# Kernel optimization log

Measured on AMD Instinct MI355X. Metric: run time of the kernel, lower is better.

Reference implementation:

```python
import jax, jax.numpy as jnp
import numpy as np

WS = (2, 7, 7)   # window size (d, h, w)
NH = 4           # num heads
EPS = 1e-5       # LayerNorm eps (torch default)


def _rel_index():
    wd, wh, ww = WS
    coords = np.stack(np.meshgrid(np.arange(wd), np.arange(wh), np.arange(ww), indexing='ij'))  # (3,wd,wh,ww)
    cf = coords.reshape(3, -1)                      # (3, N)
    rel = cf[:, :, None] - cf[:, None, :]           # (3, N, N)
    rel = rel.transpose(1, 2, 0).astype(np.int64)   # (N, N, 3)
    rel[..., 0] += wd - 1
    rel[..., 1] += wh - 1
    rel[..., 2] += ww - 1
    rel[..., 0] *= (2 * wh - 1) * (2 * ww - 1)
    rel[..., 1] *= (2 * ww - 1)
    return jnp.asarray(rel.sum(-1), dtype=jnp.int32)  # (N, N)


def setup_inputs() -> dict:
    key = jax.random.key(0)
    ks = jax.random.split(key, 6)
    C, CH = 128, 512
    TBL = (2 * WS[0] - 1) * (2 * WS[1] - 1) * (2 * WS[2] - 1)  # 507
    rn = lambda k, s, sc=0.02: jax.random.normal(k, s, jnp.float32) * sc
    return {
        'x': jax.random.normal(ks[0], (2, 8, 56, 56, C), jnp.float32),
        'norm1_w': jnp.ones((C,), jnp.float32), 'norm1_b': jnp.zeros((C,), jnp.float32),
        'qkv_w': rn(ks[1], (3 * C, C)), 'qkv_b': jnp.zeros((3 * C,), jnp.float32),
        'bias_table': rn(ks[2], (TBL, NH)),
        'proj_w': rn(ks[3], (C, C)), 'proj_b': jnp.zeros((C,), jnp.float32),
        'norm2_w': jnp.ones((C,), jnp.float32), 'norm2_b': jnp.zeros((C,), jnp.float32),
        'fc1_w': rn(ks[4], (CH, C)), 'fc1_b': jnp.zeros((CH,), jnp.float32),
        'fc2_w': rn(ks[5], (C, CH)), 'fc2_b': jnp.zeros((C,), jnp.float32),
        'rel_index': _rel_index(),
    }


def _layernorm(x, w, b):
    m = jnp.mean(x, axis=-1, keepdims=True)
    v = jnp.mean(jnp.square(x - m), axis=-1, keepdims=True)
    return (x - m) * jax.lax.rsqrt(v + EPS) * w + b


def reference(x, norm1_w, norm1_b, qkv_w, qkv_b, bias_table, proj_w, proj_b,
              norm2_w, norm2_b, fc1_w, fc1_b, fc2_w, fc2_b, rel_index):
    B, D, H, W, C = x.shape
    wd, wh, ww = WS
    N = wd * wh * ww
    hd = C // NH

    shortcut = x
    xn = _layernorm(x, norm1_w, norm1_b)
    # window partition: (B,D,H,W,C) -> (B*nW, N, C)
    xw = xn.reshape(B, D // wd, wd, H // wh, wh, W // ww, ww, C)
    xw = xw.transpose(0, 1, 3, 5, 2, 4, 6, 7).reshape(-1, N, C)
    B_ = xw.shape[0]

    qkv = (xw @ qkv_w.T + qkv_b).reshape(B_, N, 3, NH, hd).transpose(2, 0, 3, 1, 4)
    q, k, v = qkv[0] * (hd ** -0.5), qkv[1], qkv[2]   # (B_, NH, N, hd)
    attn = jnp.einsum('bhnd,bhmd->bhnm', q, k)
    bias = bias_table[rel_index.reshape(-1)].reshape(N, N, NH).transpose(2, 0, 1)  # (NH,N,N)
    attn = jax.nn.softmax(attn + bias[None], axis=-1)
    out = jnp.einsum('bhnm,bhmd->bhnd', attn, v).transpose(0, 2, 1, 3).reshape(B_, N, C)
    out = out @ proj_w.T + proj_b

    # window reverse: (B*nW, N, C) -> (B,D,H,W,C)
    xr = out.reshape(B, D // wd, H // wh, W // ww, wd, wh, ww, C)
    xr = xr.transpose(0, 1, 4, 2, 5, 3, 6, 7).reshape(B, D, H, W, C)

    x = shortcut + xr
    h = _layernorm(x, norm2_w, norm2_b)
    h = jax.nn.gelu(h @ fc1_w.T + fc1_b, approximate=False)  # torch nn.GELU = exact erf
    return x + (h @ fc2_w.T + fc2_b)
```

## Files before the change

kernel.cpp:

```cpp
#include <hip/hip_runtime.h>
#include <hip/hip_bf16.h>

typedef __hip_bfloat16 bf16;
typedef unsigned short u16t;
typedef unsigned int u32t;
typedef __attribute__((ext_vector_type(8))) short bf16x8_t;
typedef __attribute__((ext_vector_type(4))) float f32x4_t;

#define DEVI static __device__ __forceinline__

DEVI float u2f(u32t bits) { union { u32t u; float f; } v; v.u = bits; return v.f; }
DEVI float bflo(u32t u) { return u2f((u & 0xffffu) << 16); }
DEVI float bfhi(u32t u) { return u2f(u & 0xffff0000u); }
DEVI float sh2f(short s) { return u2f(((u32t)(u16t)s) << 16); }
DEVI float bf2f(bf16 h) { return __bfloat162float(h); }
DEVI bf16 f2bf(float f) { return __float2bfloat16(f); }
DEVI u16t f2bfbits(float f) {
  bf16 h = __float2bfloat16(f);
  union { bf16 h; u16t u; } v; v.h = h; return v.u;
}

DEVI void gl_lds16(const void* g, void* l) {
  __builtin_amdgcn_global_load_lds(
      (const __attribute__((address_space(1))) unsigned int*)g,
      (__attribute__((address_space(3))) unsigned int*)l, 16, 0, 0);
}

#define TOK   50176
#define NWIN  512
#define NTOK  98
#define NHEAD 4
#define HDIM  32
#define QSCALE 0.17677669529663687f

__global__ __launch_bounds__(256) void cvt4_k(
    const float* __restrict__ a, const float* __restrict__ b,
    const float* __restrict__ c, const float* __restrict__ d,
    bf16* __restrict__ o) {
  int i = blockIdx.x * 256 + threadIdx.x;
  const float* s; int off;
  if (i < 49152)       { s = a; off = 0; }
  else if (i < 65536)  { s = b; off = 49152; }
  else if (i < 131072) { s = c; off = 65536; }
  else                 { s = d; off = 131072; }
  float v = s[i - off];
  if (i < 16384) v *= QSCALE;
  o[i] = f2bf(v);
}

__global__ __launch_bounds__(256) void bias_k(const float* __restrict__ btab,
                                              const int* __restrict__ relidx,
                                              const float* __restrict__ qkv_b,
                                              float* __restrict__ BmatT,
                                              float* __restrict__ bsc) {
  int idx = blockIdx.x * 256 + threadIdx.x;
  if (idx < NTOK * NTOK) {
    int i = idx / NTOK, j = idx - i * NTOK;
    int r = relidx[idx] * NHEAD;
#pragma unroll
    for (int h = 0; h < NHEAD; h++)
      BmatT[(size_t)(h * NTOK + j) * 112 + i] = btab[r + h];
  }
  if (blockIdx.x == 0 && threadIdx.x < 384)
    bsc[threadIdx.x] = qkv_b[threadIdx.x] * (threadIdx.x < 128 ? QSCALE : 1.0f);
}

__global__ __launch_bounds__(256) void ln1_k(
    const float* __restrict__ x, const float* __restrict__ w,
    const float* __restrict__ b, bf16* __restrict__ o)
{
  const int wave = threadIdx.x >> 6, lane = threadIdx.x & 63;
  const int t = blockIdx.x * 4 + wave;
  const int c = lane << 1;
  float2 xv = *(const float2*)(x + (size_t)t * 128 + c);
  float x0 = xv.x, x1 = xv.y;
  float s = x0 + x1, ss = x0 * x0 + x1 * x1;
#pragma unroll
  for (int m = 32; m; m >>= 1) { s += __shfl_xor(s, m); ss += __shfl_xor(ss, m); }
  float mean = s * 0.0078125f;
  float var = ss * 0.0078125f - mean * mean;
  float rstd = rsqrtf(var + 1e-5f);
  float y0 = (x0 - mean) * rstd * w[c]     + b[c];
  float y1 = (x1 - mean) * rstd * w[c + 1] + b[c + 1];
  int wi = t % 56; int r = t / 56;
  int hi_ = r % 56; r /= 56;
  int di = r & 7; int bi = r >> 3;
  int nw = ((bi * 4 + (di >> 1)) * 8 + hi_ / 7) * 8 + wi / 7;
  int n  = ((di & 1) * 7 + hi_ % 7) * 7 + wi % 7;
  u32t ov = ((u32t)f2bfbits(y1) << 16) | (u32t)f2bfbits(y0);
  *(u32t*)((u16t*)o + (size_t)(nw * NTOK + n) * 128 + c) = ov;
}

DEVI int winrev(int grow) {
  int nw = grow / NTOK, n = grow - nw * NTOK;
  int wq = nw & 7, hq = (nw >> 3) & 7, dq = (nw >> 6) & 3, bb = nw >> 8;
  int wr = n % 7; int q7 = n / 7; int hr = q7 % 7, dr = q7 / 7;
  return ((bb * 8 + dq * 2 + dr) * 56 + hq * 7 + hr) * 56 + wq * 7 + wr;
}

template <int MODE, int NT16, int KT>
__global__ __launch_bounds__(256) void gemm3_k(
    const bf16* __restrict__ A, const bf16* __restrict__ W,
    const float* __restrict__ bias, const float* __restrict__ resX,
    const bf16* __restrict__ resB2, bf16* __restrict__ outB,
    bf16* __restrict__ outB2, float* __restrict__ outF,
    const float* __restrict__ lnw, const float* __restrict__ lnb, int N)
{
  __shared__ __align__(16) short As[128 * 128];
  __shared__ __align__(16) short Bs[NT16 * 16 * 128];
  const int K = KT * 128;
  const int tid = threadIdx.x;
  const int rowBase = blockIdx.y << 7;
  const int colBase = blockIdx.x * (NT16 * 16);
  const int wv = tid >> 6, lane = tid & 63;
  const int q = lane >> 4, r16 = lane & 15;
  const int mB = wv << 5;

  f32x4_t acc[2][NT16];
#pragma unroll
  for (int i = 0; i < 2; i++)
#pragma unroll
    for (int j = 0; j < NT16; j++) acc[i][j] = (f32x4_t){0.f, 0.f, 0.f, 0.f};

#pragma unroll
  for (int kt = 0; kt < KT; kt++) {
    const int kc = kt << 7;
#pragma unroll
    for (int t = 0; t < 8; t++) {
      int f = tid + (t << 8);
      int row = f >> 4, cs = (f & 15) ^ (row & 15);
      gl_lds16((const u16t*)A + (size_t)(rowBase + row) * K + kc + (cs << 3),
               &As[f << 3]);
    }
#pragma unroll
    for (int t = 0; t < NT16; t++) {
      int f = tid + (t << 8);
      int row = f >> 4, cs = (f & 15) ^ (row & 15);
      gl_lds16((const u16t*)W + (size_t)(colBase + row) * K + kc + (cs << 3),
               &Bs[f << 3]);
    }
    __syncthreads();
#pragma unroll
    for (int ks = 0; ks < 4; ks++) {
      bf16x8_t af[2], bfr[NT16];
#pragma unroll
      for (int mt = 0; mt < 2; mt++) {
        int row = mB + (mt << 4) + r16;
        int slot = ((ks << 2) + q) ^ (row & 15);
        af[mt] = *(const bf16x8_t*)&As[(row << 7) + (slot << 3)];
      }
#pragma unroll
      for (int nt = 0; nt < NT16; nt++) {
        int row = (nt << 4) + r16;
        int slot = ((ks << 2) + q) ^ (row & 15);
        bfr[nt] = *(const bf16x8_t*)&Bs[(row << 7) + (slot << 3)];
      }
#pragma unroll
      for (int mt = 0; mt < 2; mt++)
#pragma unroll
        for (int nt = 0; nt < NT16; nt++)
          acc[mt][nt] = __builtin_amdgcn_mfma_f32_16x16x32_bf16(
              af[mt], bfr[nt], acc[mt][nt], 0, 0, 0);
    }
    __syncthreads();
  }

  float bv[NT16];
#pragma unroll
  for (int nt = 0; nt < NT16; nt++) bv[nt] = bias[colBase + (nt << 4) + r16];

  if (MODE == 1) {
#pragma unroll
    for (int mt = 0; mt < 2; mt++)
#pragma unroll
      for (int reg = 0; reg < 4; reg++) {
        int lrow = mB + (mt << 4) + (q << 2) + reg;
#pragma unroll
        for (int nt = 0; nt < NT16; nt++)
          As[(lrow << 7) + (nt << 4) + r16] = (short)f2bfbits(acc[mt][nt][reg] + bv[nt]);
      }
    __syncthreads();
#pragma unroll
    for (int t = 0; t < 8; t++) {
      int f = tid + (t << 8);
      int row = f >> 4, c8 = (f & 15) << 3;
      int tt = winrev(rowBase + row);
      size_t ob = (size_t)tt * 128 + c8;
      float4 r0 = *(const float4*)(resX + ob);
      float4 r1 = *(const float4*)(resX + ob + 4);
      short* cs = &As[(row << 7) + c8];
      u16t pk[8];
      pk[0] = f2bfbits(sh2f(cs[0]) + r0.x); pk[1] = f2bfbits(sh2f(cs[1]) + r0.y);
      pk[2] = f2bfbits(sh2f(cs[2]) + r0.z); pk[3] = f2bfbits(sh2f(cs[3]) + r0.w);
      pk[4] = f2bfbits(sh2f(cs[4]) + r1.x); pk[5] = f2bfbits(sh2f(cs[5]) + r1.y);
      pk[6] = f2bfbits(sh2f(cs[6]) + r1.z); pk[7] = f2bfbits(sh2f(cs[7]) + r1.w);
      *(uint4*)((u16t*)outB + ob) = *(const uint4*)pk;
      *(uint4*)cs = *(const uint4*)pk;
    }
    __syncthreads();
    const int c = lane << 1;
    float2 lw = *(const float2*)(lnw + c);
    float2 lb = *(const float2*)(lnb + c);
#pragma unroll 4
    for (int rr = 0; rr < 32; rr++) {
      int row = (wv << 5) + rr;
      u32t u = *(const u32t*)&As[(row << 7) + c];
      float x0 = bflo(u), x1 = bfhi(u);
      float s = x0 + x1, ss = x0 * x0 + x1 * x1;
#pragma unroll
      for (int m = 32; m; m >>= 1) { s += __shfl_xor(s, m); ss += __shfl_xor(ss, m); }
      float mean = s * 0.0078125f;
      float var = ss * 0.0078125f - mean * mean;
      float rstd = rsqrtf(var + 1e-5f);
      float y0 = (x0 - mean) * rstd * lw.x + lb.x;
      float y1 = (x1 - mean) * rstd * lw.y + lb.y;
      int tt = winrev(rowBase + row);
      u32t ov = ((u32t)f2bfbits(y1) << 16) | (u32t)f2bfbits(y0);
      *(u32t*)((u16t*)outB2 + (size_t)tt * 128 + c) = ov;
    }
    return;
  }

#pragma unroll
  for (int mt = 0; mt < 2; mt++)
#pragma unroll
    for (int reg = 0; reg < 4; reg++) {
      int lrow = mB + (mt << 4) + (q << 2) + reg;
#pragma unroll
      for (int nt = 0; nt < NT16; nt++) {
        float v = acc[mt][nt][reg] + bv[nt];
        As[(lrow << 6) + (nt << 4) + r16] = (short)f2bfbits(v);
      }
    }
  __syncthreads();
#pragma unroll
  for (int t = 0; t < 4; t++) {
    int f = tid + (t << 8);
    int row = f >> 3, c8 = (f & 7) << 3;
    size_t ob = (size_t)(rowBase + row) * N + colBase + c8;
    *(uint4*)((u16t*)outB + ob) = *(const uint4*)&As[(row << 6) + c8];
  }
}

__global__ __launch_bounds__(256, 2) void mlp_fused_k(
    const bf16* __restrict__ Axn, const bf16* __restrict__ F1,
    const bf16* __restrict__ F2, const float* __restrict__ b1,
    const float* __restrict__ b2, const bf16* __restrict__ resB,
    float* __restrict__ out)
{
  __shared__ __align__(16) char smem[81920];
  short* As  = (short*)smem;
  short* F1s = (short*)(smem + 32768);
  short* F2s = (short*)(smem + 49152);
  short* Hs  = (short*)(smem + 65536);
  float* Cf  = (float*)smem;

  const int tid = threadIdx.x;
  const int rowBase = blockIdx.x << 7;
  const int wv = tid >> 6, lane = tid & 63;
  const int q = lane >> 4, r16 = lane & 15;
  const int mB = wv << 5;

#pragma unroll
  for (int t = 0; t < 8; t++) {
    int f = tid + (t << 8);
    int row = f >> 4, cs = (f & 15) ^ (row & 15);
    gl_lds16((const u16t*)Axn + (size_t)(rowBase + row) * 128 + (cs << 3),
             &As[f << 3]);
  }
#pragma unroll
  for (int t = 0; t < 4; t++) {
    int f = tid + (t << 8);
    int row = f >> 4, cs = (f & 15) ^ (row & 15);
    gl_lds16((const u16t*)F1 + (size_t)row * 128 + (cs << 3), &F1s[f << 3]);
  }
#pragma unroll
  for (int t = 0; t < 4; t++) {
    int f = tid + (t << 8);
    int row = f >> 3, cs = (f & 7) ^ (row & 7);
    gl_lds16((const u16t*)F2 + (size_t)row * 512 + (cs << 3), &F2s[f << 3]);
  }
  __syncthreads();

  f32x4_t oacc[2][8];
#pragma unroll
  for (int i = 0; i < 2; i++)
#pragma unroll
    for (int j = 0; j < 8; j++) oacc[i][j] = (f32x4_t){0.f, 0.f, 0.f, 0.f};

#pragma unroll 1
  for (int c = 0; c < 8; c++) {
    if (c > 0) {
#pragma unroll
      for (int t = 0; t < 4; t++) {
        int f = tid + (t << 8);
        int row = f >> 4, cs = (f & 15) ^ (row & 15);
        gl_lds16((const u16t*)F1 + (size_t)(c * 64 + row) * 128 + (cs << 3),
                 &F1s[f << 3]);
      }
#pragma unroll
      for (int t = 0; t < 4; t++) {
        int f = tid + (t << 8);
        int row = f >> 3, cs = (f & 7) ^ (row & 7);
        gl_lds16((const u16t*)F2 + (size_t)row * 512 + c * 64 + (cs << 3),
                 &F2s[f << 3]);
      }
      __syncthreads();
    }

    f32x4_t hacc[2][4];
#pragma unroll
    for (int i = 0; i < 2; i++)
#pragma unroll
      for (int j = 0; j < 4; j++) hacc[i][j] = (f32x4_t){0.f, 0.f, 0.f, 0.f};
#pragma unroll
    for (int ks = 0; ks < 4; ks++) {
      bf16x8_t af[2], bfr[4];
#pragma unroll
      for (int mt = 0; mt < 2; mt++) {
        int row = mB + (mt << 4) + r16;
        int slot = ((ks << 2) + q) ^ (row & 15);
        af[mt] = *(const bf16x8_t*)&As[(row << 7) + (slot << 3)];
      }
#pragma unroll
      for (int nt = 0; nt < 4; nt++) {
        int row = (nt << 4) + r16;
        int slot = ((ks << 2) + q) ^ (row & 15);
        bfr[nt] = *(const bf16x8_t*)&F1s[(row << 7) + (slot << 3)];
      }
#pragma unroll
      for (int mt = 0; mt < 2; mt++)
#pragma unroll
        for (int nt = 0; nt < 4; nt++)
          hacc[mt][nt] = __builtin_amdgcn_mfma_f32_16x16x32_bf16(
              af[mt], bfr[nt], hacc[mt][nt], 0, 0, 0);
    }

    float bb[4];
#pragma unroll
    for (int nt = 0; nt < 4; nt++) bb[nt] = b1[c * 64 + (nt << 4) + r16];
#pragma unroll
    for (int mt = 0; mt < 2; mt++)
#pragma unroll
      for (int reg = 0; reg < 4; reg++) {
        int lrow = mB + (mt << 4) + (q << 2) + reg;
#pragma unroll
        for (int nt = 0; nt < 4; nt++) {
          float v = hacc[mt][nt][reg] + bb[nt];
          v = 0.5f * v * (1.0f + erff(v * 0.70710678118654752f));
          int col = (nt << 4) + r16;
          int sp = (col >> 3) ^ (lrow & 7);
          Hs[(lrow << 6) + (sp << 3) + (col & 7)] = (short)f2bfbits(v);
        }
      }
    __syncthreads();

#pragma unroll
    for (int ks = 0; ks < 2; ks++) {
      bf16x8_t af[2], bfr[8];
#pragma unroll
      for (int mt = 0; mt < 2; mt++) {
        int row = mB + (mt << 4) + r16;
        int slot = ((ks << 2) + q) ^ (row & 7);
        af[mt] = *(const bf16x8_t*)&Hs[(row << 6) + (slot << 3)];
      }
#pragma unroll
      for (int nt = 0; nt < 8; nt++) {
        int row = (nt << 4) + r16;
        int slot = ((ks << 2) + q) ^ (row & 7);
        bfr[nt] = *(const bf16x8_t*)&F2s[(row << 6) + (slot << 3)];
      }
#pragma unroll
      for (int mt = 0; mt < 2; mt++)
#pragma unroll
        for (int nt = 0; nt < 8; nt++)
          oacc[mt][nt] = __builtin_amdgcn_mfma_f32_16x16x32_bf16(
              af[mt], bfr[nt], oacc[mt][nt], 0, 0, 0);
    }
    __syncthreads();
  }

  float bv[8];
#pragma unroll
  for (int nt = 0; nt < 8; nt++) bv[nt] = b2[(nt << 4) + r16];
#pragma unroll
  for (int mt = 0; mt < 2; mt++)
#pragma unroll
    for (int reg = 0; reg < 4; reg++) {
      int lrow = mB + (mt << 4) + (q << 2) + reg;
#pragma unroll
      for (int nt = 0; nt < 8; nt++)
        Cf[lrow * 132 + (nt << 4) + r16] = oacc[mt][nt][reg] + bv[nt];
    }
  __syncthreads();
#pragma unroll
  for (int t = 0; t < 16; t++) {
    int f = tid + (t << 8);
    int row = f >> 5, c4 = (f & 31) << 2;
    size_t ob = (size_t)(rowBase + row) * 128 + c4;
    const u16t* rp = (const u16t*)resB + ob;
    const float* cp = &Cf[row * 132 + c4];
    float4 v;
    v.x = cp[0] + sh2f(rp[0]);
    v.y = cp[1] + sh2f(rp[1]);
    v.z = cp[2] + sh2f(rp[2]);
    v.w = cp[3] + sh2f(rp[3]);
    *(float4*)(out + ob) = v;
  }
}

#define PSTR 136
__global__ __launch_bounds__(256) void attn_mfma_k(
    const bf16* __restrict__ qkv, const float* __restrict__ BmatT,
    bf16* __restrict__ out)
{
  __shared__ short Vt[32 * PSTR];
  __shared__ short Ps[112 * PSTR];
  const int nw = blockIdx.x, h = blockIdx.y;
  const int tid = threadIdx.x;
  const int wv = tid >> 6, lane = tid & 63;
  const int q = lane >> 4, r16 = lane & 15;

  for (int idx = tid; idx < 32 * 38; idx += 256) {
    int d = idx / 38, j = 98 + idx % 38;
    Vt[d * PSTR + j] = 0;
  }
  for (int idx = tid; idx < 112 * 12; idx += 256) {
    int r = idx / 12, c = (idx % 12) << 1;
    *(u32t*)&Ps[r * PSTR + 112 + c] = 0;
  }
  for (int idx = tid; idx < NTOK * 16; idx += 256) {
    int j = idx >> 4, d2 = (idx & 15) << 1;
    u32t uv = *(const u32t*)((const u16t*)qkv +
                             (size_t)(nw * NTOK + j) * 384 + 256 + h * 32 + d2);
    Vt[d2 * PSTR + j] = (short)(uv & 0xffffu);
    Vt[(d2 + 1) * PSTR + j] = (short)(uv >> 16);
  }
  __syncthreads();

  const int mt0 = wv;
  const bool has2 = (wv + 4) < 7;
  const int mt1 = has2 ? wv + 4 : wv;

  int i0 = mt0 * 16 + r16; if (i0 > NTOK - 1) i0 = NTOK - 1;
  int i1 = mt1 * 16 + r16; if (i1 > NTOK - 1) i1 = NTOK - 1;
  bf16x8_t aq0 = *(const bf16x8_t*)((const u16t*)qkv +
      (size_t)(nw * NTOK + i0) * 384 + h * 32 + (q << 3));
  bf16x8_t aq1 = *(const bf16x8_t*)((const u16t*)qkv +
      (size_t)(nw * NTOK + i1) * 384 + h * 32 + (q << 3));

  f32x4_t sc[2][7];
#pragma unroll
  for (int nt = 0; nt < 7; nt++) {
    int j = (nt << 4) + r16; if (j > NTOK - 1) j = NTOK - 1;
    const float* bRow = &BmatT[(size_t)(h * NTOK + j) * 112];
    bf16x8_t bk = *(const bf16x8_t*)((const u16t*)qkv +
        (size_t)(nw * NTOK + j) * 384 + 128 + h * 32 + (q << 3));
    f32x4_t b0 = *(const f32x4_t*)&bRow[mt0 * 16 + (q << 2)];
    f32x4_t b1 = *(const f32x4_t*)&bRow[mt1 * 16 + (q << 2)];
    sc[0][nt] = __builtin_amdgcn_mfma_f32_16x16x32_bf16(aq0, bk, b0, 0, 0, 0);
    sc[1][nt] = __builtin_amdgcn_mfma_f32_16x16x32_bf16(aq1, bk, b1, 0, 0, 0);
  }

#pragma unroll
  for (int sel = 0; sel < 2; sel++) {
    if (sel == 1 && !has2) break;
    int mtile = sel ? mt1 : mt0;
    int ibase = mtile * 16 + (q << 2);
    float s[4][7];
#pragma unroll
    for (int nt = 0; nt < 7; nt++) {
      int j = (nt << 4) + r16;
#pragma unroll
      for (int reg = 0; reg < 4; reg++) {
        int i = ibase + reg;
        s[reg][nt] = (i < NTOK && j < NTOK) ? sc[sel][nt][reg] : -1.0e30f;
      }
    }
#pragma unroll
    for (int reg = 0; reg < 4; reg++) {
      float m = -3.0e38f;
#pragma unroll
      for (int nt = 0; nt < 7; nt++) m = fmaxf(m, s[reg][nt]);
#pragma unroll
      for (int d = 8; d; d >>= 1) m = fmaxf(m, __shfl_xor(m, d));
      float sum = 0.f;
#pragma unroll
      for (int nt = 0; nt < 7; nt++) { s[reg][nt] = __expf(s[reg][nt] - m); sum += s[reg][nt]; }
#pragma unroll
      for (int d = 8; d; d >>= 1) sum += __shfl_xor(sum, d);
      float inv = 1.f / sum;
#pragma unroll
      for (int nt = 0; nt < 7; nt++)
        Ps[(ibase + reg) * PSTR + (nt << 4) + r16] =
            (short)f2bfbits(s[reg][nt] * inv);
    }
    f32x4_t o0 = {0.f, 0.f, 0.f, 0.f}, o1 = {0.f, 0.f, 0.f, 0.f};
#pragma unroll
    for (int kt = 0; kt < 4; kt++) {
      bf16x8_t ap = *(const bf16x8_t*)&Ps[(mtile * 16 + r16) * PSTR + (kt << 5) + (q << 3)];
      bf16x8_t bv0 = *(const bf16x8_t*)&Vt[r16 * PSTR + (kt << 5) + (q << 3)];
      bf16x8_t bv1 = *(const bf16x8_t*)&Vt[(16 + r16) * PSTR + (kt << 5) + (q << 3)];
      o0 = __builtin_amdgcn_mfma_f32_16x16x32_bf16(ap, bv0, o0, 0, 0, 0);
      o1 = __builtin_amdgcn_mfma_f32_16x16x32_bf16(ap, bv1, o1, 0, 0, 0);
    }
#pragma unroll
    for (int reg = 0; reg < 4; reg++) {
      int i = mtile * 16 + (q << 2) + reg;
      if (i < NTOK) {
        size_t ob = (size_t)(nw * NTOK + i) * 128 + h * 32;
        out[ob + r16] = f2bf(o0[reg]);
        out[ob + 16 + r16] = f2bf(o1[reg]);
      }
    }
  }
}

extern "C" void kernel_launch(void* const* d_in, const int* in_sizes, int n_in,
                              void* d_out, int out_size, void* d_ws, size_t ws_size,
                              hipStream_t stream) {
  const float* x      = (const float*)d_in[0];
  const float* n1w    = (const float*)d_in[1];
  const float* n1b    = (const float*)d_in[2];
  const float* qkv_w  = (const float*)d_in[3];
  const float* qkv_b  = (const float*)d_in[4];
  const float* btab   = (const float*)d_in[5];
  const float* proj_w = (const float*)d_in[6];
  const float* proj_b = (const float*)d_in[7];
  const float* n2w    = (const float*)d_in[8];
  const float* n2b    = (const float*)d_in[9];
  const float* fc1_w  = (const float*)d_in[10];
  const float* fc1_b  = (const float*)d_in[11];
  const float* fc2_w  = (const float*)d_in[12];
  const float* fc2_b  = (const float*)d_in[13];
  const int*   relidx = (const int*)d_in[14];

  const size_t Asz = (size_t)TOK * 128 * 2;
  char* ws = (char*)d_ws;
  bf16* wbf   = (bf16*)ws;
  bf16* qkvw16  = wbf;
  bf16* projw16 = wbf + 49152;
  bf16* fc1w16  = wbf + 65536;
  bf16* fc2w16  = wbf + 131072;
  float* BmatT = (float*)(ws + 393216);
  float* bsc   = (float*)(ws + 393216 + 175616);
  char* R = ws + (1 << 20);
  bf16* xw    = (bf16*)d_out;
  bf16* attn  = (bf16*)d_out;
  bf16* qkv   = (bf16*)R;
  bf16* x2    = (bf16*)R;
  bf16* xn2   = (bf16*)(R + Asz);
  float* out  = (float*)d_out;

  cvt4_k<<<768, 256, 0, stream>>>(qkv_w, proj_w, fc1_w, fc2_w, wbf);
  bias_k<<<38, 256, 0, stream>>>(btab, relidx, qkv_b, BmatT, bsc);
  ln1_k<<<TOK / 4, 256, 0, stream>>>(x, n1w, n1b, xw);
  gemm3_k<0, 4, 1><<<dim3(6, TOK / 128), 256, 0, stream>>>(
      xw, qkvw16, bsc, nullptr, nullptr, qkv, nullptr, nullptr,
      nullptr, nullptr, 384);
  attn_mfma_k<<<dim3(NWIN, NHEAD), 256, 0, stream>>>(qkv, BmatT, attn);
  gemm3_k<1, 8, 1><<<dim3(1, TOK / 128), 256, 0, stream>>>(
      attn, projw16, proj_b, x, nullptr, x2, xn2, nullptr, n2w, n2b, 128);
  mlp_fused_k<<<TOK / 128, 256, 0, stream>>>(
      xn2, fc1w16, fc2w16, fc1_b, fc2_b, x2, out);
}
```

Before: 218.3 us.

## Fuse QKV projection GEMM into per-window attention kernel

Replaces the separate QKV GEMM kernel and the per-(window, head) attention kernel with one kernel per window. That kernel computes the QKV projection for the window's 98 tokens into LDS, with XOR-swizzled layouts and double-buffered weight tiles, then loops over the four heads for attention. This removes the global write and read-back of the qkv intermediate and one launch. In exchange it needs about 157KB of LDS per block, which allows one block per CU, and the grid has 4x fewer blocks.

```diff
diff --git a/kernel.cpp b/kernel.cpp
--- a/kernel.cpp
+++ b/kernel.cpp
@@ -242,6 +242,192 @@
   }
 }
 
+#define PSTR 136
+__global__ __launch_bounds__(256) void qkvattn_k(
+    const bf16* xw, const bf16* __restrict__ Wq,
+    const float* __restrict__ bsc, const float* __restrict__ BmatT,
+    bf16* out)
+{
+  __shared__ __align__(16) char smem[160768];
+  short* QK  = (short*)smem;
+  short* Vt  = (short*)(smem + 50176);
+  short* As  = (short*)(smem + 82944);
+  short* Ps  = (short*)(smem + 82944);
+  short* Bs0 = (short*)(smem + 111616);
+  short* Bs1 = (short*)(smem + 136192);
+
+  const int nw = blockIdx.x;
+  const int tid = threadIdx.x;
+  const int wv = tid >> 6, lane = tid & 63;
+  const int q = lane >> 4, r16 = lane & 15;
+  const int rt0 = wv, rt1 = wv + 4;
+
+  for (int idx = tid; idx < 128 * 30; idx += 256) {
+    int d = idx / 30, j = 98 + idx % 30;
+    Vt[d * 128 + ((((j >> 3) ^ (d & 15))) << 3) + (j & 7)] = 0;
+  }
+#pragma unroll
+  for (int t = 0; t < 7; t++) {
+    int f = tid + (t << 8);
+    if (f < 1568) {
+      int row = f >> 4, cs = (f & 15) ^ (row & 15);
+      gl_lds16((const u16t*)xw + (size_t)(nw * NTOK + row) * 128 + (cs << 3),
+               &As[f << 3]);
+    }
+  }
+#pragma unroll
+  for (int t = 0; t < 6; t++) {
+    int f = tid + (t << 8);
+    int row = f >> 4, cs = (f & 15) ^ (row & 15);
+    gl_lds16((const u16t*)Wq + (size_t)row * 128 + (cs << 3), &Bs0[f << 3]);
+  }
+  __syncthreads();
+
+#pragma unroll 1
+  for (int qt = 0; qt < 4; qt++) {
+    short* Bcur = (qt & 1) ? Bs1 : Bs0;
+    if (qt < 3) {
+      short* Bnxt = (qt & 1) ? Bs0 : Bs1;
+#pragma unroll
+      for (int t = 0; t < 6; t++) {
+        int f = tid + (t << 8);
+        int row = f >> 4, cs = (f & 15) ^ (row & 15);
+        gl_lds16((const u16t*)Wq + (size_t)((qt + 1) * 96 + row) * 128 + (cs << 3),
+                 &Bnxt[f << 3]);
+      }
+    }
+    f32x4_t acc[2][6];
+#pragma unroll
+    for (int i = 0; i < 2; i++)
+#pragma unroll
+      for (int j = 0; j < 6; j++) acc[i][j] = (f32x4_t){0.f, 0.f, 0.f, 0.f};
+#pragma unroll
+    for (int ks = 0; ks < 4; ks++) {
+      bf16x8_t af[2], bfr[6];
+#pragma unroll
+      for (int mt = 0; mt < 2; mt++) {
+        int row = ((mt ? rt1 : rt0) << 4) + r16;
+        int slot = ((ks << 2) + q) ^ (row & 15);
+        af[mt] = *(const bf16x8_t*)&As[(row << 7) + (slot << 3)];
+      }
+#pragma unroll
+      for (int nt = 0; nt < 6; nt++) {
+        int row = (nt << 4) + r16;
+        int slot = ((ks << 2) + q) ^ (row & 15);
+        bfr[nt] = *(const bf16x8_t*)&Bcur[(row << 7) + (slot << 3)];
+      }
+#pragma unroll
+      for (int mt = 0; mt < 2; mt++)
+#pragma unroll
+        for (int nt = 0; nt < 6; nt++)
+          acc[mt][nt] = __builtin_amdgcn_mfma_f32_16x16x32_bf16(
+              af[mt], bfr[nt], acc[mt][nt], 0, 0, 0);
+    }
+#pragma unroll
+    for (int mt = 0; mt < 2; mt++)
+#pragma unroll
+      for (int reg = 0; reg < 4; reg++) {
+        int row = ((mt ? rt1 : rt0) << 4) + (q << 2) + reg;
+        if (row < NTOK) {
+#pragma unroll
+          for (int nt = 0; nt < 6; nt++) {
+            int cg = qt * 96 + (nt << 4) + r16;
+            u16t bits = f2bfbits(acc[mt][nt][reg] + bsc[cg]);
+            if (cg < 256) {
+              QK[(row << 8) + (((cg >> 3) ^ (row & 15)) << 3) + (cg & 7)] =
+                  (short)bits;
+            } else {
+              int d = cg - 256;
+              Vt[(d << 7) + (((row >> 3) ^ (d & 15)) << 3) + (row & 7)] =
+                  (short)bits;
+            }
+          }
+        }
+      }
+    __syncthreads();
+  }
+
+  for (int idx = tid; idx < 128 * 12; idx += 256) {
+    int r = idx / 12, c = (idx % 12) << 1;
+    *(u32t*)&Ps[r * PSTR + 112 + c] = 0;
+  }
+  __syncthreads();
+
+#pragma unroll 1
+  for (int h = 0; h < NHEAD; h++) {
+    const int i0 = (rt0 << 4) + r16, i1 = (rt1 << 4) + r16;
+    const int gq = (h << 2) + q, gk = 16 + (h << 2) + q;
+    bf16x8_t aq0 = *(const bf16x8_t*)&QK[(i0 << 8) + ((gq ^ (i0 & 15)) << 3)];
+    bf16x8_t aq1 = *(const bf16x8_t*)&QK[(i1 << 8) + ((gq ^ (i1 & 15)) << 3)];
+
+    f32x4_t sc[2][7];
+#pragma unroll
+    for (int nt = 0; nt < 7; nt++) {
+      int j = (nt << 4) + r16;
+      int jc = j > NTOK - 1 ? NTOK - 1 : j;
+      const float* bRow = &BmatT[(size_t)(h * NTOK + jc) * 112];
+      bf16x8_t bk = *(const bf16x8_t*)&QK[(j << 8) + ((gk ^ (j & 15)) << 3)];
+      f32x4_t b0 = *(const f32x4_t*)&bRow[(rt0 << 4) + (q << 2)];
+      f32x4_t b1 = *(const f32x4_t*)&bRow[(rt1 << 4) + (q << 2)];
+      sc[0][nt] = __builtin_amdgcn_mfma_f32_16x16x32_bf16(aq0, bk, b0, 0, 0, 0);
+      sc[1][nt] = __builtin_amdgcn_mfma_f32_16x16x32_bf16(aq1, bk, b1, 0, 0, 0);
+    }
+
+#pragma unroll
+    for (int sel = 0; sel < 2; sel++) {
+      int mtile = sel ? rt1 : rt0;
+      int ibase = (mtile << 4) + (q << 2);
+      float s[4][7];
+#pragma unroll
+      for (int nt = 0; nt < 7; nt++) {
+        int j = (nt << 4) + r16;
+#pragma unroll
+        for (int reg = 0; reg < 4; reg++) {
+          int i = ibase + reg;
+          s[reg][nt] = (i < NTOK && j < NTOK) ? sc[sel][nt][reg] : -1.0e30f;
+        }
+      }
+#pragma unroll
+      for (int reg = 0; reg < 4; reg++) {
+        float m = -3.0e38f;
+#pragma unroll
+        for (int nt = 0; nt < 7; nt++) m = fmaxf(m, s[reg][nt]);
+#pragma unroll
+        for (int d = 8; d; d >>= 1) m = fmaxf(m, __shfl_xor(m, d));
+        float sum = 0.f;
+#pragma unroll
+        for (int nt = 0; nt < 7; nt++) { s[reg][nt] = __expf(s[reg][nt] - m); sum += s[reg][nt]; }
+#pragma unroll
+        for (int d = 8; d; d >>= 1) sum += __shfl_xor(sum, d);
+        float inv = 1.f / sum;
+#pragma unroll
+        for (int nt = 0; nt < 7; nt++)
+          Ps[(ibase + reg) * PSTR + (nt << 4) + r16] =
+              (short)f2bfbits(s[reg][nt] * inv);
+      }
+      f32x4_t o0 = {0.f, 0.f, 0.f, 0.f}, o1 = {0.f, 0.f, 0.f, 0.f};
+#pragma unroll
+      for (int kt = 0; kt < 4; kt++) {
+        int g = (kt << 2) + q;
+        bf16x8_t ap = *(const bf16x8_t*)&Ps[((mtile << 4) + r16) * PSTR + (kt << 5) + (q << 3)];
+        bf16x8_t bv0 = *(const bf16x8_t*)&Vt[(((h << 5) + r16) << 7) + ((g ^ r16) << 3)];
+        bf16x8_t bv1 = *(const bf16x8_t*)&Vt[(((h << 5) + 16 + r16) << 7) + ((g ^ r16) << 3)];
+        o0 = __builtin_amdgcn_mfma_f32_16x16x32_bf16(ap, bv0, o0, 0, 0, 0);
+        o1 = __builtin_amdgcn_mfma_f32_16x16x32_bf16(ap, bv1, o1, 0, 0, 0);
+      }
+#pragma unroll
+      for (int reg = 0; reg < 4; reg++) {
+        int i = ibase + reg;
+        if (i < NTOK) {
+          size_t ob = (size_t)(nw * NTOK + i) * 128 + (h << 5);
+          out[ob + r16] = f2bf(o0[reg]);
+          out[ob + 16 + r16] = f2bf(o1[reg]);
+        }
+      }
+    }
+  }
+}
+
 __global__ __launch_bounds__(256, 2) void mlp_fused_k(
     const bf16* __restrict__ Axn, const bf16* __restrict__ F1,
     const bf16* __restrict__ F2, const float* __restrict__ b1,
@@ -406,113 +592,6 @@
     v.z = cp[2] + sh2f(rp[2]);
     v.w = cp[3] + sh2f(rp[3]);
     *(float4*)(out + ob) = v;
-  }
-}
-
-#define PSTR 136
-__global__ __launch_bounds__(256) void attn_mfma_k(
-    const bf16* __restrict__ qkv, const float* __restrict__ BmatT,
-    bf16* __restrict__ out)
-{
-  __shared__ short Vt[32 * PSTR];
-  __shared__ short Ps[112 * PSTR];
-  const int nw = blockIdx.x, h = blockIdx.y;
-  const int tid = threadIdx.x;
-  const int wv = tid >> 6, lane = tid & 63;
-  const int q = lane >> 4, r16 = lane & 15;
-
-  for (int idx = tid; idx < 32 * 38; idx += 256) {
-    int d = idx / 38, j = 98 + idx % 38;
-    Vt[d * PSTR + j] = 0;
-  }
-  for (int idx = tid; idx < 112 * 12; idx += 256) {
-    int r = idx / 12, c = (idx % 12) << 1;
-    *(u32t*)&Ps[r * PSTR + 112 + c] = 0;
-  }
-  for (int idx = tid; idx < NTOK * 16; idx += 256) {
-    int j = idx >> 4, d2 = (idx & 15) << 1;
-    u32t uv = *(const u32t*)((const u16t*)qkv +
-                             (size_t)(nw * NTOK + j) * 384 + 256 + h * 32 + d2);
-    Vt[d2 * PSTR + j] = (short)(uv & 0xffffu);
-    Vt[(d2 + 1) * PSTR + j] = (short)(uv >> 16);
-  }
-  __syncthreads();
-
-  const int mt0 = wv;
-  const bool has2 = (wv + 4) < 7;
-  const int mt1 = has2 ? wv + 4 : wv;
-
-  int i0 = mt0 * 16 + r16; if (i0 > NTOK - 1) i0 = NTOK - 1;
-  int i1 = mt1 * 16 + r16; if (i1 > NTOK - 1) i1 = NTOK - 1;
-  bf16x8_t aq0 = *(const bf16x8_t*)((const u16t*)qkv +
-      (size_t)(nw * NTOK + i0) * 384 + h * 32 + (q << 3));
-  bf16x8_t aq1 = *(const bf16x8_t*)((const u16t*)qkv +
-      (size_t)(nw * NTOK + i1) * 384 + h * 32 + (q << 3));
-
-  f32x4_t sc[2][7];
-#pragma unroll
-  for (int nt = 0; nt < 7; nt++) {
-    int j = (nt << 4) + r16; if (j > NTOK - 1) j = NTOK - 1;
-    const float* bRow = &BmatT[(size_t)(h * NTOK + j) * 112];
-    bf16x8_t bk = *(const bf16x8_t*)((const u16t*)qkv +
-        (size_t)(nw * NTOK + j) * 384 + 128 + h * 32 + (q << 3));
-    f32x4_t b0 = *(const f32x4_t*)&bRow[mt0 * 16 + (q << 2)];
-    f32x4_t b1 = *(const f32x4_t*)&bRow[mt1 * 16 + (q << 2)];
-    sc[0][nt] = __builtin_amdgcn_mfma_f32_16x16x32_bf16(aq0, bk, b0, 0, 0, 0);
-    sc[1][nt] = __builtin_amdgcn_mfma_f32_16x16x32_bf16(aq1, bk, b1, 0, 0, 0);
-  }
-
-#pragma unroll
-  for (int sel = 0; sel < 2; sel++) {
-    if (sel == 1 && !has2) break;
-    int mtile = sel ? mt1 : mt0;
-    int ibase = mtile * 16 + (q << 2);
-    float s[4][7];
-#pragma unroll
-    for (int nt = 0; nt < 7; nt++) {
-      int j = (nt << 4) + r16;
-#pragma unroll
-      for (int reg = 0; reg < 4; reg++) {
-        int i = ibase + reg;
-        s[reg][nt] = (i < NTOK && j < NTOK) ? sc[sel][nt][reg] : -1.0e30f;
-      }
-    }
-#pragma unroll
-    for (int reg = 0; reg < 4; reg++) {
-      float m = -3.0e38f;
-#pragma unroll
-      for (int nt = 0; nt < 7; nt++) m = fmaxf(m, s[reg][nt]);
-#pragma unroll
-      for (int d = 8; d; d >>= 1) m = fmaxf(m, __shfl_xor(m, d));
-      float sum = 0.f;
-#pragma unroll
-      for (int nt = 0; nt < 7; nt++) { s[reg][nt] = __expf(s[reg][nt] - m); sum += s[reg][nt]; }
-#pragma unroll
-      for (int d = 8; d; d >>= 1) sum += __shfl_xor(sum, d);
-      float inv = 1.f / sum;
-#pragma unroll
-      for (int nt = 0; nt < 7; nt++)
-        Ps[(ibase + reg) * PSTR + (nt << 4) + r16] =
-            (short)f2bfbits(s[reg][nt] * inv);
-    }
-    f32x4_t o0 = {0.f, 0.f, 0.f, 0.f}, o1 = {0.f, 0.f, 0.f, 0.f};
-#pragma unroll
-    for (int kt = 0; kt < 4; kt++) {
-      bf16x8_t ap = *(const bf16x8_t*)&Ps[(mtile * 16 + r16) * PSTR + (kt << 5) + (q << 3)];
-      bf16x8_t bv0 = *(const bf16x8_t*)&Vt[r16 * PSTR + (kt << 5) + (q << 3)];
-      bf16x8_t bv1 = *(const bf16x8_t*)&Vt[(16 + r16) * PSTR + (kt << 5) + (q << 3)];
-      o0 = __builtin_amdgcn_mfma_f32_16x16x32_bf16(ap, bv0, o0, 0, 0, 0);
-      o1 = __builtin_amdgcn_mfma_f32_16x16x32_bf16(ap, bv1, o1, 0, 0, 0);
-    }
-#pragma unroll
-    for (int reg = 0; reg < 4; reg++) {
-      int i = mtile * 16 + (q << 2) + reg;
-      if (i < NTOK) {
-        size_t ob = (size_t)(nw * NTOK + i) * 128 + h * 32;
-        out[ob + r16] = f2bf(o0[reg]);
-        out[ob + 16 + r16] = f2bf(o1[reg]);
-      }
-    }
   }
 }
 
@@ -547,7 +626,6 @@
   char* R = ws + (1 << 20);
   bf16* xw    = (bf16*)d_out;
   bf16* attn  = (bf16*)d_out;
-  bf16* qkv   = (bf16*)R;
   bf16* x2    = (bf16*)R;
   bf16* xn2   = (bf16*)(R + Asz);
   float* out  = (float*)d_out;
@@ -555,10 +633,7 @@
   cvt4_k<<<768, 256, 0, stream>>>(qkv_w, proj_w, fc1_w, fc2_w, wbf);
   bias_k<<<38, 256, 0, stream>>>(btab, relidx, qkv_b, BmatT, bsc);
   ln1_k<<<TOK / 4, 256, 0, stream>>>(x, n1w, n1b, xw);
-  gemm3_k<0, 4, 1><<<dim3(6, TOK / 128), 256, 0, stream>>>(
-      xw, qkvw16, bsc, nullptr, nullptr, qkv, nullptr, nullptr,
-      nullptr, nullptr, 384);
-  attn_mfma_k<<<dim3(NWIN, NHEAD), 256, 0, stream>>>(qkv, BmatT, attn);
+  qkvattn_k<<<NWIN, 256, 0, stream>>>(xw, qkvw16, bsc, BmatT, attn);
   gemm3_k<1, 8, 1><<<dim3(1, TOK / 128), 256, 0, stream>>>(
       attn, projw16, proj_b, x, nullptr, x2, xn2, nullptr, n2w, n2b, 128);
   mlp_fused_k<<<TOK / 128, 256, 0, stream>>>(
```

Measured after the change: 249.1 us. +14.1%, slower.
